# Kernel optimization log

Measured on AMD Instinct MI355X. Metric: run time of the kernel, lower is better.

## Reference

```python
import jax, jax.numpy as jnp
import numpy as np

B, P, J, MOT, K, NB, WN, H = 64, 12273, 80, 94, 64, 20, 17, 128
W_POSE = 1.0

def euler_to_rotmat(a):
    # a: [..., 3] radians, R = Rz @ Ry @ Rx
    sx, sy, sz = jnp.sin(a[..., 0]), jnp.sin(a[..., 1]), jnp.sin(a[..., 2])
    cx, cy, cz = jnp.cos(a[..., 0]), jnp.cos(a[..., 1]), jnp.cos(a[..., 2])
    r00 = cz * cy; r01 = cz * sy * sx - sz * cx; r02 = cz * sy * cx + sz * sx
    r10 = sz * cy; r11 = sz * sy * sx + cz * cx; r12 = sz * sy * cx - cz * sx
    r20 = -sy;     r21 = cy * sx;                r22 = cy * cx
    return jnp.stack([jnp.stack([r00, r01, r02], -1),
                      jnp.stack([r10, r11, r12], -1),
                      jnp.stack([r20, r21, r22], -1)], -2)

def setup_inputs() -> dict:
    key = jax.random.key(0)
    ks = jax.random.split(key, 20)
    f32 = jnp.float32
    return {
        'in_pc_batch': jax.random.normal(ks[0], (B, P, 3), f32),
        't_nor': jax.random.normal(ks[1], (B, P, 3), f32),
        'rest_verts': jax.random.normal(ks[2], (P, 3), f32),
        'skin_weights': jax.random.uniform(ks[3], (P, J), f32),
        'mul_weight_list': jax.random.normal(ks[4], (J, MOT), f32),
        'query': jax.random.normal(ks[5], (B, J, 3), f32),
        'cloth_pose_std': jax.random.uniform(ks[6], (3,), f32),
        'cloth_pose_mean': jax.random.normal(ks[7], (3,), f32),
        'cloth_trans_std': jax.random.uniform(ks[8], (3,), f32),
        'cloth_trans_mean': jax.random.normal(ks[9], (3,), f32),
        'W1': jax.random.normal(ks[10], (3 + K, H), f32) * 0.1,
        'b1': jnp.zeros((H,), f32),
        'W2': jax.random.normal(ks[11], (H, 6), f32) * 0.1,
        'b2': jnp.zeros((6,), f32),
        'tmtemp': jax.random.normal(ks[12], (B, MOT, K), f32),
        'Wd': jax.random.normal(ks[13], (MOT * K, NB * WN), f32) * 0.02,
        'bd': jnp.zeros((NB * WN,), f32),
        'DPSD': jax.random.normal(ks[14], (NB, WN, P, 3), f32) * 0.1,
        'ssdr_res_std': jax.random.uniform(ks[15], (3,), f32),
        'ssdr_res_mean': jax.random.normal(ks[16], (3,), f32),
    }

def reference(in_pc_batch, t_nor, rest_verts, skin_weights, mul_weight_list,
              query, cloth_pose_std, cloth_pose_mean, cloth_trans_std,
              cloth_trans_mean, W1, b1, W2, b2, tmtemp, Wd, bd, DPSD,
              ssdr_res_std, ssdr_res_mean):
    # per-joint field input: [B, J, K]
    field_input = jnp.einsum('bjk,lj->blk', tmtemp, jax.nn.relu(mul_weight_list))
    # FieldNet: per-joint MLP on concat(query, field_input) -> [B, J, 6]
    h = jnp.concatenate([query, field_input], axis=-1)
    pred_rt = jax.nn.relu(h @ W1 + b1) @ W2 + b2
    pred_pose = pred_rt[..., 0:3] * cloth_pose_std + cloth_pose_mean
    pred_trans = (query + pred_rt[..., 3:6]) * cloth_trans_std + cloth_trans_mean
    # detailsnet + fused 20-basis accumulation: [B, P, 3]
    nbat = tmtemp.shape[0]
    detailkey = (tmtemp.reshape(nbat, -1) @ Wd + bd).reshape(nbat, NB, WN)
    detail_res = jnp.einsum('bnw,nwpx->bpx', detailkey, DPSD)
    detail_res = detail_res * ssdr_res_std + ssdr_res_mean
    # SSDR LBS skinning with Euler-angle rotations (degrees -> radians)
    R = euler_to_rotmat(jnp.deg2rad(pred_pose))            # [B, J, 3, 3]
    skinned = (jnp.einsum('pj,bjxy,py->bpx', skin_weights, R, rest_verts)
               + jnp.einsum('pj,bjx->bpx', skin_weights, pred_trans))
    out_pc = skinned + detail_res                          # [B, P, 3]
    loss_pose_l1 = jnp.mean(jnp.abs(in_pc_batch[:, :, 0:3] - out_pc))
    loss = loss_pose_l1 * W_POSE + 1e-4 * jnp.mean(DPSD ** 2)
    return loss[None], out_pc
```

## Files before the change

kernel.cpp:

```cpp
#include <hip/hip_runtime.h>

#define B_   64
#define P_   12273
#define J_   80
#define MOT_ 94
#define K_   64
#define H_   128
#define Q_   340
#define NE_  36819
#define MK_  6016
#define PW_  12288

typedef float v4f  __attribute__((ext_vector_type(4)));
typedef float v8f  __attribute__((ext_vector_type(8)));
typedef float v16f __attribute__((ext_vector_type(16)));
#define AS4 __attribute__((address_space(4)))

__device__ __forceinline__ const AS4 float* unif(const float* p){
  return (const AS4 float*)(unsigned long long)p;
}
__device__ __forceinline__ const AS4 v4f* univ4(const float* p){
  return (const AS4 v4f*)(unsigned long long)p;
}
__device__ __forceinline__ const AS4 v8f* univ8(const float* p){
  return (const AS4 v8f*)(unsigned long long)p;
}
__device__ __forceinline__ const AS4 v16f* univ16(const float* p){
  return (const AS4 v16f*)(unsigned long long)p;
}

__global__ __launch_bounds__(256) void k_prep(
    const float* __restrict__ query, const float* __restrict__ mwl,
    const float* __restrict__ tm,    const float* __restrict__ W1,
    const float* __restrict__ b1,    const float* __restrict__ W2,
    const float* __restrict__ b2,    const float* __restrict__ cps,
    const float* __restrict__ cpm,   const float* __restrict__ cts,
    const float* __restrict__ ctm,   const float* __restrict__ skin,
    float* __restrict__ G,           float* __restrict__ tm_t,
    float* __restrict__ w_t,         float* __restrict__ lacc)
{
  __shared__ float smem[80 * 65];
  int blk = blockIdx.x;
  int t = threadIdx.x;
  if (blk < 1280){
    int lane = t & 63;
    int wid = __builtin_amdgcn_readfirstlane(t >> 6);
    int bj = blk * 4 + wid;
    int b = bj / J_, l = bj - b * J_;
    float* hs = smem + wid * 80;
    float acc = 0.f;
    const AS4 float* mp = unif(mwl + l * MOT_);
    const float* tp = tm + (size_t)b * MK_ + lane;
    #pragma unroll 2
    for (int j = 0; j < MOT_; j++){
      float w = mp[j]; w = w > 0.f ? w : 0.f;
      acc = fmaf(w, tp[j * K_], acc);
    }
    hs[3 + lane] = acc;
    if (lane < 3) hs[lane] = query[(size_t)bj * 3 + lane];
    __syncthreads();
    float a1 = b1[lane], a2 = b1[lane + 64];
    for (int i = 0; i < 3 + K_; i++){
      float hv = hs[i];
      a1 = fmaf(hv, W1[i * H_ + lane], a1);
      a2 = fmaf(hv, W1[i * H_ + 64 + lane], a2);
    }
    a1 = a1 > 0.f ? a1 : 0.f;
    a2 = a2 > 0.f ? a2 : 0.f;
    const AS4 float* b2c = unif(b2);
    float rt[6];
    #pragma unroll
    for (int o = 0; o < 6; o++){
      float po = fmaf(a1, W2[lane * 6 + o], a2 * W2[(lane + 64) * 6 + o]);
      #pragma unroll
      for (int off = 32; off; off >>= 1) po += __shfl_xor(po, off);
      rt[o] = po + b2c[o];
    }
    const float D2R = 0.017453292519943295f;
    float ax = fmaf(rt[0], cps[0], cpm[0]) * D2R;
    float ay = fmaf(rt[1], cps[1], cpm[1]) * D2R;
    float az = fmaf(rt[2], cps[2], cpm[2]) * D2R;
    float tx = fmaf(hs[0] + rt[3], cts[0], ctm[0]);
    float ty = fmaf(hs[1] + rt[4], cts[1], ctm[1]);
    float tz = fmaf(hs[2] + rt[5], cts[2], ctm[2]);
    float sx, cx, sy, cy, sz, cz;
    sincosf(ax, &sx, &cx); sincosf(ay, &sy, &cy); sincosf(az, &sz, &cz);
    if (lane == 0){
      float4 r0 = make_float4(cz*cy, cz*sy*sx - sz*cx, cz*sy*cx + sz*sx, tx);
      float4 r1 = make_float4(sz*cy, sz*sy*sx + cz*cx, sz*sy*cx - cz*sx, ty);
      float4 r2 = make_float4(-sy,   cy*sx,            cy*cx,            tz);
      float4* g = (float4*)(G + (size_t)bj * 12);
      g[0] = r0; g[1] = r1; g[2] = r2;
    }
  } else if (blk < 1374){
    int m0 = (blk - 1280) * 64;
    int ml = t & 63, g = t >> 6;
    #pragma unroll
    for (int r = 0; r < 16; r++){
      int b = g * 16 + r;
      smem[ml * 65 + b] = tm[(size_t)b * MK_ + m0 + ml];
    }
    __syncthreads();
    int bl = t & 63;
    #pragma unroll
    for (int r = 0; r < 16; r++){
      int m = g * 16 + r;
      tm_t[(size_t)(m0 + m) * 64 + bl] = smem[m * 65 + bl];
    }
  } else if (blk < 1566){
    int p0 = (blk - 1374) * 64;
    #pragma unroll
    for (int k = 0; k < 20; k++){
      int idx = k * 256 + t;
      int pl = idx / 80, j = idx - pl * 80;
      int p = p0 + pl;
      smem[j * 65 + pl] = (p < P_) ? skin[(size_t)p * J_ + j] : 0.f;
    }
    __syncthreads();
    #pragma unroll
    for (int k = 0; k < 20; k++){
      int idx = k * 256 + t;
      int j = idx >> 6, pl = idx & 63;
      w_t[(size_t)j * PW_ + p0 + pl] = smem[j * 65 + pl];
    }
  } else {
    if (t < 2) lacc[t] = 0.f;
  }
}

__global__ __launch_bounds__(256) void k_dkey(
    const float* __restrict__ tm_t, const float* __restrict__ Wd,
    float* __restrict__ part, int chunk)
{
  int t = threadIdx.x;
  int lane = t & 63;
  int wid = __builtin_amdgcn_readfirstlane(t >> 6);
  int qt = blockIdx.x;
  int q = qt * 64 + lane;
  bool vq = q < Q_;
  int m0 = (blockIdx.y * 4 + wid) * chunk;
  float acc[64];
  #pragma unroll
  for (int i = 0; i < 64; i++) acc[i] = 0.f;
  const AS4 v16f* tr = univ16(tm_t);
  for (int m = m0; m < m0 + chunk; m++){
    float wd = vq ? Wd[(size_t)m * Q_ + q] : 0.f;
    v16f t0 = tr[m * 4 + 0];
    v16f t1 = tr[m * 4 + 1];
    v16f t2 = tr[m * 4 + 2];
    v16f t3 = tr[m * 4 + 3];
    #pragma unroll
    for (int i = 0; i < 16; i++){
      acc[i]      = fmaf(t0[i], wd, acc[i]);
      acc[16 + i] = fmaf(t1[i], wd, acc[16 + i]);
      acc[32 + i] = fmaf(t2[i], wd, acc[32 + i]);
      acc[48 + i] = fmaf(t3[i], wd, acc[48 + i]);
    }
  }
  __shared__ float red[4 * 64 * 64];
  float* rw = red + wid * 4096;
  #pragma unroll
  for (int i = 0; i < 64; i++) rw[i * 64 + lane] = acc[i];
  __syncthreads();
  float* pb = part + ((size_t)blockIdx.y * 6 + qt) * 4096;
  #pragma unroll
  for (int k = 0; k < 16; k++){
    int i = t + 256 * k;
    pb[i] = red[i] + red[4096 + i] + red[8192 + i] + red[12288 + i];
  }
}

__global__ __launch_bounds__(256) void k_dkred(
    const float* __restrict__ part, const float* __restrict__ bd,
    float* __restrict__ dk_t, int S)
{
  int j = blockIdx.x * 256 + threadIdx.x;
  if (j >= B_ * Q_) return;
  int b = j / Q_;
  int q = j - b * Q_;
  int qt = q >> 6, ql = q & 63;
  const float* pp = part + (size_t)qt * 4096 + b * 64 + ql;
  const size_t ST = 6 * 4096;
  float s0 = 0.f, s1 = 0.f, s2 = 0.f, s3 = 0.f;
  float s4 = 0.f, s5 = 0.f, s6 = 0.f, s7 = 0.f;
  int sy = 0;
  for (; sy + 8 <= S; sy += 8){
    s0 += pp[(sy + 0) * ST]; s1 += pp[(sy + 1) * ST];
    s2 += pp[(sy + 2) * ST]; s3 += pp[(sy + 3) * ST];
    s4 += pp[(sy + 4) * ST]; s5 += pp[(sy + 5) * ST];
    s6 += pp[(sy + 6) * ST]; s7 += pp[(sy + 7) * ST];
  }
  for (; sy < S; sy++) s0 += pp[(size_t)sy * ST];
  dk_t[q * 64 + b] = bd[q] + (((s0 + s1) + (s2 + s3)) + ((s4 + s5) + (s6 + s7)));
}

__global__ __launch_bounds__(512) void k_detail(
    const float* __restrict__ DPSD, const float* __restrict__ dk_t,
    const float* __restrict__ rstd, const float* __restrict__ rmean,
    float* __restrict__ out, float* __restrict__ lacc)
{
  int t = threadIdx.x;
  int lane = t & 63;
  int wid = __builtin_amdgcn_readfirstlane(t >> 6);
  int b0 = wid * 8;
  int e = blockIdx.x * 64 + lane;
  bool ve = e < NE_;
  const AS4 v8f* dkv = univ8(dk_t + b0);
  float acc[8];
  #pragma unroll
  for (int i = 0; i < 8; i++) acc[i] = 0.f;
  float sq = 0.f;
  const float* Dp = DPSD + e;
  for (int q0 = 0; q0 < Q_; q0 += 4){
    float d0 = ve ? Dp[(size_t)(q0 + 0) * NE_] : 0.f;
    float d1 = ve ? Dp[(size_t)(q0 + 1) * NE_] : 0.f;
    float d2 = ve ? Dp[(size_t)(q0 + 2) * NE_] : 0.f;
    float d3 = ve ? Dp[(size_t)(q0 + 3) * NE_] : 0.f;
    v8f r0 = dkv[(q0 + 0) * 8];
    v8f r1 = dkv[(q0 + 1) * 8];
    v8f r2 = dkv[(q0 + 2) * 8];
    v8f r3 = dkv[(q0 + 3) * 8];
    if (wid == 0){
      sq = fmaf(d0, d0, sq); sq = fmaf(d1, d1, sq);
      sq = fmaf(d2, d2, sq); sq = fmaf(d3, d3, sq);
    }
    #pragma unroll
    for (int i = 0; i < 8; i++){
      acc[i] = fmaf(r0[i], d0, acc[i]);
      acc[i] = fmaf(r1[i], d1, acc[i]);
      acc[i] = fmaf(r2[i], d2, acc[i]);
      acc[i] = fmaf(r3[i], d3, acc[i]);
    }
  }
  if (ve){
    int x = e % 3;
    float s = rstd[x], m = rmean[x];
    #pragma unroll
    for (int i = 0; i < 8; i++)
      out[1 + (size_t)(b0 + i) * NE_ + e] = fmaf(acc[i], s, m);
  }
  if (wid == 0){
    #pragma unroll
    for (int off = 32; off; off >>= 1) sq += __shfl_xor(sq, off);
    if (lane == 0) atomicAdd(&lacc[1], sq);
  }
}

__global__ __launch_bounds__(256) void k_skin(
    const float* __restrict__ G, const float* __restrict__ w_t,
    const float* __restrict__ rest, const float* __restrict__ in_pc,
    float* __restrict__ out, float* __restrict__ lacc)
{
  int t = threadIdx.x;
  int lane = t & 63;
  int wid = __builtin_amdgcn_readfirstlane(t >> 6);
  int p  = blockIdx.x * 64 + lane;
  int bA = blockIdx.y * 8 + wid * 2;
  const AS4 v4f* gA = univ4(G + (size_t)bA * J_ * 12);
  const AS4 v4f* gB = univ4(G + ((size_t)bA + 1) * J_ * 12);
  float accA[12], accB[12];
  #pragma unroll
  for (int c = 0; c < 12; c++){ accA[c] = 0.f; accB[c] = 0.f; }
  const float* wp = w_t + p;
  #pragma unroll 4
  for (int j = 0; j < J_; j++){
    float w = wp[(size_t)j * PW_];
    v4f a0 = gA[j * 3 + 0], a1 = gA[j * 3 + 1], a2 = gA[j * 3 + 2];
    v4f c0 = gB[j * 3 + 0], c1 = gB[j * 3 + 1], c2 = gB[j * 3 + 2];
    #pragma unroll
    for (int c = 0; c < 4; c++){
      accA[c]     = fmaf(w, a0[c], accA[c]);
      accA[4 + c] = fmaf(w, a1[c], accA[4 + c]);
      accA[8 + c] = fmaf(w, a2[c], accA[8 + c]);
      accB[c]     = fmaf(w, c0[c], accB[c]);
      accB[4 + c] = fmaf(w, c1[c], accB[4 + c]);
      accB[8 + c] = fmaf(w, c2[c], accB[8 + c]);
    }
  }
  bool vp = p < P_;
  float vx = 0.f, vy = 0.f, vz = 0.f;
  if (vp){ vx = rest[p * 3]; vy = rest[p * 3 + 1]; vz = rest[p * 3 + 2]; }
  float lsum = 0.f;
  if (vp){
    size_t baseA = ((size_t)bA * P_ + p) * 3;
    size_t baseB = baseA + (size_t)P_ * 3;
    #pragma unroll
    for (int x = 0; x < 3; x++){
      float v = fmaf(accA[x*4+0], vx, fmaf(accA[x*4+1], vy, fmaf(accA[x*4+2], vz, accA[x*4+3])));
      v += out[1 + baseA + x];
      lsum += fabsf(in_pc[baseA + x] - v);
      out[1 + baseA + x] = v;
    }
    #pragma unroll
    for (int x = 0; x < 3; x++){
      float v = fmaf(accB[x*4+0], vx, fmaf(accB[x*4+1], vy, fmaf(accB[x*4+2], vz, accB[x*4+3])));
      v += out[1 + baseB + x];
      lsum += fabsf(in_pc[baseB + x] - v);
      out[1 + baseB + x] = v;
    }
  }
  #pragma unroll
  for (int off = 32; off; off >>= 1) lsum += __shfl_xor(lsum, off);
  __shared__ float red[4];
  if (lane == 0) red[wid] = lsum;
  __syncthreads();
  if (t == 0) atomicAdd(&lacc[0], red[0] + red[1] + red[2] + red[3]);
}

__global__ void k_finalize(const float* __restrict__ lacc, float* __restrict__ out){
  if (threadIdx.x == 0 && blockIdx.x == 0){
    float loss = lacc[0] * (1.f / 2356416.f) + 1e-4f * (lacc[1] * (1.f / 12518460.f));
    out[0] = loss;
  }
}

extern "C" void kernel_launch(void* const* d_in, const int* in_sizes, int n_in,
                              void* d_out, int out_size, void* d_ws, size_t ws_size,
                              hipStream_t stream){
  const float* in_pc = (const float*)d_in[0];
  const float* rest  = (const float*)d_in[2];
  const float* skin  = (const float*)d_in[3];
  const float* mwl   = (const float*)d_in[4];
  const float* query = (const float*)d_in[5];
  const float* cps   = (const float*)d_in[6];
  const float* cpm   = (const float*)d_in[7];
  const float* cts   = (const float*)d_in[8];
  const float* ctm   = (const float*)d_in[9];
  const float* W1    = (const float*)d_in[10];
  const float* b1    = (const float*)d_in[11];
  const float* W2    = (const float*)d_in[12];
  const float* b2    = (const float*)d_in[13];
  const float* tm    = (const float*)d_in[14];
  const float* Wd    = (const float*)d_in[15];
  const float* bd    = (const float*)d_in[16];
  const float* DPSD  = (const float*)d_in[17];
  const float* rstd  = (const float*)d_in[18];
  const float* rmean = (const float*)d_in[19];
  float* out = (float*)d_out;

  float* ws   = (float*)d_ws;
  float* G    = ws;
  float* dk_t = ws + 61440;
  float* lacc = ws + 61440 + 21760;
  float* tm_t = ws + 83204;
  float* w_t  = ws + 83204 + 385024;
  float* part = ws + 83204 + 385024 + 983040;

  size_t fixed = 83204 + 385024 + 983040;
  int S = 16;
  if (ws_size >= (fixed + (size_t)94 * 24576) * 4) S = 94;
  else if (ws_size >= (fixed + (size_t)47 * 24576) * 4) S = 47;
  int chunk = MK_ / (S * 4);

  k_prep    <<<1567, 256, 0, stream>>>(query, mwl, tm, W1, b1, W2, b2,
                                       cps, cpm, cts, ctm, skin,
                                       G, tm_t, w_t, lacc);
  k_dkey    <<<dim3(6, S), 256, 0, stream>>>(tm_t, Wd, part, chunk);
  k_dkred   <<<85, 256, 0, stream>>>(part, bd, dk_t, S);
  k_detail  <<<576, 512, 0, stream>>>(DPSD, dk_t, rstd, rmean, out, lacc);
  k_skin    <<<dim3(192, 8), 256, 0, stream>>>(G, w_t, rest, in_pc, out, lacc);
  k_finalize<<<1, 64, 0, stream>>>(lacc, out);
}
```

Before: 283.3 us.

## Split detail contraction over basis halves, restructure detail-key GEMM and reduction

The detail kernel's 340-term basis reduction is split across two grid slices. One slice writes a staging buffer and the other writes the output, and the skinning kernel sums both and applies the std/mean scaling. This doubles the number of workgroups streaming DPSD, and register prefetch of the next group of DPSD rows is added. k_dkey now gives each wave 16 of the 64 batch columns over a fixed 64-row chunk with software-pipelined loads, which drops the shared-memory reduction. k_dkred uses 8 lanes per output with shuffle reductions. The costs are extra staging traffic, a fixed split count of S=94 that assumes enough workspace, and that the split is chosen by workspace size.

After: 268.4 us. -5.2%, faster.

```diff
diff --git a/kernel.cpp b/kernel.cpp
--- a/kernel.cpp
+++ b/kernel.cpp
@@ -130,7 +130,7 @@
 
 __global__ __launch_bounds__(256) void k_dkey(
     const float* __restrict__ tm_t, const float* __restrict__ Wd,
-    float* __restrict__ part, int chunk)
+    float* __restrict__ part)
 {
   int t = threadIdx.x;
   int lane = t & 63;
@@ -138,66 +138,59 @@
   int qt = blockIdx.x;
   int q = qt * 64 + lane;
   bool vq = q < Q_;
-  int m0 = (blockIdx.y * 4 + wid) * chunk;
-  float acc[64];
-  #pragma unroll
-  for (int i = 0; i < 64; i++) acc[i] = 0.f;
+  int m0 = blockIdx.y * 64;
   const AS4 v16f* tr = univ16(tm_t);
-  for (int m = m0; m < m0 + chunk; m++){
-    float wd = vq ? Wd[(size_t)m * Q_ + q] : 0.f;
-    v16f t0 = tr[m * 4 + 0];
-    v16f t1 = tr[m * 4 + 1];
-    v16f t2 = tr[m * 4 + 2];
-    v16f t3 = tr[m * 4 + 3];
-    #pragma unroll
-    for (int i = 0; i < 16; i++){
-      acc[i]      = fmaf(t0[i], wd, acc[i]);
-      acc[16 + i] = fmaf(t1[i], wd, acc[16 + i]);
-      acc[32 + i] = fmaf(t2[i], wd, acc[32 + i]);
-      acc[48 + i] = fmaf(t3[i], wd, acc[48 + i]);
-    }
-  }
-  __shared__ float red[4 * 64 * 64];
-  float* rw = red + wid * 4096;
-  #pragma unroll
-  for (int i = 0; i < 64; i++) rw[i * 64 + lane] = acc[i];
-  __syncthreads();
-  float* pb = part + ((size_t)blockIdx.y * 6 + qt) * 4096;
-  #pragma unroll
-  for (int k = 0; k < 16; k++){
-    int i = t + 256 * k;
-    pb[i] = red[i] + red[4096 + i] + red[8192 + i] + red[12288 + i];
-  }
+  float acc[16];
+  #pragma unroll
+  for (int i = 0; i < 16; i++) acc[i] = 0.f;
+  float wbuf[4];
+  #pragma unroll
+  for (int i = 0; i < 4; i++)
+    wbuf[i] = vq ? Wd[(size_t)(m0 + i) * Q_ + q] : 0.f;
+  v16f tb0 = tr[(size_t)(m0 + 0) * 4 + wid];
+  v16f tb1 = tr[(size_t)(m0 + 1) * 4 + wid];
+  #pragma unroll 4
+  for (int mm = 0; mm < 60; mm++){
+    float wd = wbuf[mm & 3];
+    wbuf[mm & 3] = vq ? Wd[(size_t)(m0 + mm + 4) * Q_ + q] : 0.f;
+    v16f tv = tb0; tb0 = tb1;
+    tb1 = tr[(size_t)(m0 + mm + 2) * 4 + wid];
+    #pragma unroll
+    for (int i = 0; i < 16; i++) acc[i] = fmaf(tv[i], wd, acc[i]);
+  }
+  #pragma unroll
+  for (int mm = 60; mm < 64; mm++){
+    float wd = wbuf[mm & 3];
+    v16f tv = tb0; tb0 = tb1;
+    if (mm < 62) tb1 = tr[(size_t)(m0 + mm + 2) * 4 + wid];
+    #pragma unroll
+    for (int i = 0; i < 16; i++) acc[i] = fmaf(tv[i], wd, acc[i]);
+  }
+  float* pb = part + ((size_t)blockIdx.y * 6 + qt) * 4096 + (size_t)(wid * 16) * 64;
+  #pragma unroll
+  for (int i = 0; i < 16; i++) pb[i * 64 + lane] = acc[i];
 }
 
 __global__ __launch_bounds__(256) void k_dkred(
     const float* __restrict__ part, const float* __restrict__ bd,
     float* __restrict__ dk_t, int S)
 {
-  int j = blockIdx.x * 256 + threadIdx.x;
-  if (j >= B_ * Q_) return;
-  int b = j / Q_;
-  int q = j - b * Q_;
+  int t = threadIdx.x;
+  int jj = blockIdx.x * 32 + (t >> 3);
+  int dl = t & 7;
+  int b = jj / Q_, q = jj - b * Q_;
   int qt = q >> 6, ql = q & 63;
   const float* pp = part + (size_t)qt * 4096 + b * 64 + ql;
-  const size_t ST = 6 * 4096;
-  float s0 = 0.f, s1 = 0.f, s2 = 0.f, s3 = 0.f;
-  float s4 = 0.f, s5 = 0.f, s6 = 0.f, s7 = 0.f;
-  int sy = 0;
-  for (; sy + 8 <= S; sy += 8){
-    s0 += pp[(sy + 0) * ST]; s1 += pp[(sy + 1) * ST];
-    s2 += pp[(sy + 2) * ST]; s3 += pp[(sy + 3) * ST];
-    s4 += pp[(sy + 4) * ST]; s5 += pp[(sy + 5) * ST];
-    s6 += pp[(sy + 6) * ST]; s7 += pp[(sy + 7) * ST];
-  }
-  for (; sy < S; sy++) s0 += pp[(size_t)sy * ST];
-  dk_t[q * 64 + b] = bd[q] + (((s0 + s1) + (s2 + s3)) + ((s4 + s5) + (s6 + s7)));
+  float s = 0.f;
+  for (int d = dl; d < S; d += 8) s += pp[(size_t)d * 6 * 4096];
+  s += __shfl_xor(s, 1); s += __shfl_xor(s, 2); s += __shfl_xor(s, 4);
+  if (dl == 0) dk_t[q * 64 + b] = bd[q] + s;
 }
 
 __global__ __launch_bounds__(512) void k_detail(
     const float* __restrict__ DPSD, const float* __restrict__ dk_t,
-    const float* __restrict__ rstd, const float* __restrict__ rmean,
-    float* __restrict__ out, float* __restrict__ lacc)
+    float* __restrict__ stg0, float* __restrict__ out,
+    float* __restrict__ lacc, int qn)
 {
   int t = threadIdx.x;
   int lane = t & 63;
@@ -205,39 +198,51 @@
   int b0 = wid * 8;
   int e = blockIdx.x * 64 + lane;
   bool ve = e < NE_;
+  int q0 = blockIdx.y * qn;
   const AS4 v8f* dkv = univ8(dk_t + b0);
+  const float* Dp = DPSD + e;
   float acc[8];
   #pragma unroll
   for (int i = 0; i < 8; i++) acc[i] = 0.f;
   float sq = 0.f;
-  const float* Dp = DPSD + e;
-  for (int q0 = 0; q0 < Q_; q0 += 4){
-    float d0 = ve ? Dp[(size_t)(q0 + 0) * NE_] : 0.f;
-    float d1 = ve ? Dp[(size_t)(q0 + 1) * NE_] : 0.f;
-    float d2 = ve ? Dp[(size_t)(q0 + 2) * NE_] : 0.f;
-    float d3 = ve ? Dp[(size_t)(q0 + 3) * NE_] : 0.f;
-    v8f r0 = dkv[(q0 + 0) * 8];
-    v8f r1 = dkv[(q0 + 1) * 8];
-    v8f r2 = dkv[(q0 + 2) * 8];
-    v8f r3 = dkv[(q0 + 3) * 8];
+  float dc[5], dn[5];
+  #pragma unroll
+  for (int i = 0; i < 5; i++)
+    dc[i] = ve ? Dp[(size_t)(q0 + i) * NE_] : 0.f;
+  int ng = qn / 5;
+  for (int g = 0; g < ng; g++){
+    int qq = q0 + g * 5;
+    if (g + 1 < ng){
+      #pragma unroll
+      for (int i = 0; i < 5; i++)
+        dn[i] = ve ? Dp[(size_t)(qq + 5 + i) * NE_] : 0.f;
+    }
+    v8f r0 = dkv[(qq + 0) * 8];
+    v8f r1 = dkv[(qq + 1) * 8];
+    v8f r2 = dkv[(qq + 2) * 8];
+    v8f r3 = dkv[(qq + 3) * 8];
+    v8f r4 = dkv[(qq + 4) * 8];
     if (wid == 0){
-      sq = fmaf(d0, d0, sq); sq = fmaf(d1, d1, sq);
-      sq = fmaf(d2, d2, sq); sq = fmaf(d3, d3, sq);
+      #pragma unroll
+      for (int i = 0; i < 5; i++) sq = fmaf(dc[i], dc[i], sq);
     }
     #pragma unroll
     for (int i = 0; i < 8; i++){
-      acc[i] = fmaf(r0[i], d0, acc[i]);
-      acc[i] = fmaf(r1[i], d1, acc[i]);
-      acc[i] = fmaf(r2[i], d2, acc[i]);
-      acc[i] = fmaf(r3[i], d3, acc[i]);
-    }
+      acc[i] = fmaf(r0[i], dc[0], acc[i]);
+      acc[i] = fmaf(r1[i], dc[1], acc[i]);
+      acc[i] = fmaf(r2[i], dc[2], acc[i]);
+      acc[i] = fmaf(r3[i], dc[3], acc[i]);
+      acc[i] = fmaf(r4[i], dc[4], acc[i]);
+    }
+    #pragma unroll
+    for (int i = 0; i < 5; i++) dc[i] = dn[i];
   }
   if (ve){
-    int x = e % 3;
-    float s = rstd[x], m = rmean[x];
+    bool toOut = (blockIdx.y + 1 == gridDim.y);
+    float* dst = toOut ? (out + 1 + e) : (stg0 + e);
     #pragma unroll
     for (int i = 0; i < 8; i++)
-      out[1 + (size_t)(b0 + i) * NE_ + e] = fmaf(acc[i], s, m);
+      dst[(size_t)(b0 + i) * NE_] = acc[i];
   }
   if (wid == 0){
     #pragma unroll
@@ -249,7 +254,9 @@
 __global__ __launch_bounds__(256) void k_skin(
     const float* __restrict__ G, const float* __restrict__ w_t,
     const float* __restrict__ rest, const float* __restrict__ in_pc,
-    float* __restrict__ out, float* __restrict__ lacc)
+    const float* __restrict__ stg0, const float* __restrict__ rstd,
+    const float* __restrict__ rmean,
+    float* __restrict__ out, float* __restrict__ lacc, int two)
 {
   int t = threadIdx.x;
   int lane = t & 63;
@@ -280,21 +287,28 @@
   bool vp = p < P_;
   float vx = 0.f, vy = 0.f, vz = 0.f;
   if (vp){ vx = rest[p * 3]; vy = rest[p * 3 + 1]; vz = rest[p * 3 + 2]; }
+  float srs[3], srm[3];
+  #pragma unroll
+  for (int x = 0; x < 3; x++){ srs[x] = rstd[x]; srm[x] = rmean[x]; }
   float lsum = 0.f;
   if (vp){
     size_t baseA = ((size_t)bA * P_ + p) * 3;
     size_t baseB = baseA + (size_t)P_ * 3;
     #pragma unroll
     for (int x = 0; x < 3; x++){
+      float det = out[1 + baseA + x];
+      if (two) det += stg0[baseA + x];
       float v = fmaf(accA[x*4+0], vx, fmaf(accA[x*4+1], vy, fmaf(accA[x*4+2], vz, accA[x*4+3])));
-      v += out[1 + baseA + x];
+      v += fmaf(det, srs[x], srm[x]);
       lsum += fabsf(in_pc[baseA + x] - v);
       out[1 + baseA + x] = v;
     }
     #pragma unroll
     for (int x = 0; x < 3; x++){
+      float det = out[1 + baseB + x];
+      if (two) det += stg0[baseB + x];
       float v = fmaf(accB[x*4+0], vx, fmaf(accB[x*4+1], vy, fmaf(accB[x*4+2], vz, accB[x*4+3])));
-      v += out[1 + baseB + x];
+      v += fmaf(det, srs[x], srm[x]);
       lsum += fabsf(in_pc[baseB + x] - v);
       out[1 + baseB + x] = v;
     }
@@ -340,24 +354,23 @@
 
   float* ws   = (float*)d_ws;
   float* G    = ws;
-  float* dk_t = ws + 61440;
-  float* lacc = ws + 61440 + 21760;
-  float* tm_t = ws + 83204;
-  float* w_t  = ws + 83204 + 385024;
-  float* part = ws + 83204 + 385024 + 983040;
-
-  size_t fixed = 83204 + 385024 + 983040;
-  int S = 16;
-  if (ws_size >= (fixed + (size_t)94 * 24576) * 4) S = 94;
-  else if (ws_size >= (fixed + (size_t)47 * 24576) * 4) S = 47;
-  int chunk = MK_ / (S * 4);
+  float* dk_t = G + 61440;
+  float* lacc = dk_t + 21760;
+  float* tm_t = lacc + 64;
+  float* w_t  = tm_t + 385024;
+  float* un   = w_t + 983040;
+
+  size_t have = ws_size / 4;
+  int nqh = (have >= (size_t)(1451328 + 2356416)) ? 2 : 1;
+  int qn = Q_ / nqh;
 
   k_prep    <<<1567, 256, 0, stream>>>(query, mwl, tm, W1, b1, W2, b2,
                                        cps, cpm, cts, ctm, skin,
                                        G, tm_t, w_t, lacc);
-  k_dkey    <<<dim3(6, S), 256, 0, stream>>>(tm_t, Wd, part, chunk);
-  k_dkred   <<<85, 256, 0, stream>>>(part, bd, dk_t, S);
-  k_detail  <<<576, 512, 0, stream>>>(DPSD, dk_t, rstd, rmean, out, lacc);
-  k_skin    <<<dim3(192, 8), 256, 0, stream>>>(G, w_t, rest, in_pc, out, lacc);
+  k_dkey    <<<dim3(6, 94), 256, 0, stream>>>(tm_t, Wd, un);
+  k_dkred   <<<680, 256, 0, stream>>>(un, bd, dk_t, 94);
+  k_detail  <<<dim3(576, nqh), 512, 0, stream>>>(DPSD, dk_t, un, out, lacc, qn);
+  k_skin    <<<dim3(192, 8), 256, 0, stream>>>(G, w_t, rest, in_pc, un, rstd, rmean,
+                                               out, lacc, nqh - 1);
   k_finalize<<<1, 64, 0, stream>>>(lacc, out);
 }
```
